# Performance work log

Measured on AMD Instinct MI355X. Metric: run time of the kernel, lower is better.

## Reference

```python
import jax, jax.numpy as jnp
import numpy as np

N_HEADS = 16
ROPE_BASE = 10000.0
EPS = float(np.finfo(np.float32).eps)  # F.rms_norm default eps for fp32


def _rms_norm(x):
    # RMSNorm over last dim, no learned scale (modded-nanogpt `norm`)
    return x * jax.lax.rsqrt(jnp.mean(jnp.square(x), axis=-1, keepdims=True) + EPS)


def _rotary(x):
    # x: [B, T, H, D]; non-interleaved half-rotation as in the Rotary module
    B, T, H, D = x.shape
    inv_freq = (1.0 / ROPE_BASE) ** (jnp.arange(0, D, 2, dtype=jnp.float32) / D)  # [D/2]
    t = jnp.arange(T, dtype=jnp.float32)
    freqs = jnp.outer(t, inv_freq)  # [T, D/2]
    cos = jnp.cos(freqs)[None, :, None, :]
    sin = jnp.sin(freqs)[None, :, None, :]
    x1, x2 = jnp.split(x, 2, axis=3)
    y1 = x1 * cos + x2 * sin
    y2 = -x1 * sin + x2 * cos
    return jnp.concatenate((y1, y2), axis=3).astype(x.dtype)


def setup_inputs() -> dict:
    key = jax.random.key(0)
    k1, k2, k3, k4 = jax.random.split(key, 4)
    B, T, Hs = 1, 2048, 2048
    d_head = Hs // N_HEADS
    std = 0.5 * d_head ** (-0.5)
    bound = 3 ** 0.5 * std
    x = jax.random.normal(k1, (B, T, Hs), dtype=jnp.float32)
    Wqkv = jax.random.uniform(k2, (3, Hs, Hs), dtype=jnp.float32, minval=-bound, maxval=bound)
    Wo_w = jax.random.normal(k3, (Hs, Hs), dtype=jnp.float32) * (Hs ** -0.5)
    Wo_b = jax.random.normal(k4, (Hs,), dtype=jnp.float32) * 0.01
    return {"x": x, "Wqkv": Wqkv, "Wo_w": Wo_w, "Wo_b": Wo_b}


def reference(x, Wqkv, Wo_w, Wo_b):
    B, T, Hs = x.shape
    d_head = Hs // N_HEADS
    # fused QKV projection: F.linear(x, Wqkv.flatten(end_dim=1)) -> x @ W^T
    W = Wqkv.reshape(3 * Hs, Hs)
    qkv = jnp.einsum('bth,oh->bto', x, W).reshape(B, T, 3 * N_HEADS, d_head)
    q, k, v = jnp.split(qkv, 3, axis=-2)  # each [B, T, H, D]
    q, k = _rms_norm(q), _rms_norm(k)
    q, k = _rotary(q), _rotary(k)
    # causal attention (flex_attention block_mask = causal), scale = 1/sqrt(d)
    scale = 1.0 / jnp.sqrt(jnp.float32(d_head))
    scores = jnp.einsum('bthd,bshd->bhts', q, k) * scale  # [B, H, T, S]
    causal = jnp.tril(jnp.ones((T, T), dtype=bool))
    scores = jnp.where(causal[None, None], scores, jnp.float32(-1e30))
    probs = jax.nn.softmax(scores, axis=-1)
    y = jnp.einsum('bhts,bshd->bthd', probs, v).reshape(B, T, Hs)
    return jnp.einsum('bth,oh->bto', y, Wo_w) + Wo_b
```

## Files before the change

kernel.cpp:

```cpp
#include <hip/hip_runtime.h>
#include <hip/hip_bf16.h>
#include <stdint.h>

#define T_SEQ 2048
#define HS    2048
#define NH    16
#define DH    128
#define QKVN  (3*HS)

typedef __attribute__((ext_vector_type(8))) short          bf16x8;
typedef __attribute__((ext_vector_type(4))) float          f32x4;
typedef __attribute__((ext_vector_type(4))) unsigned short us4;
typedef __attribute__((ext_vector_type(8))) unsigned short us8;

__device__ __forceinline__ unsigned short f2bf(float x) {
  unsigned int u = __float_as_uint(x);
  return (unsigned short)((u + 0x7fffu + ((u >> 16) & 1u)) >> 16);
}

__device__ __forceinline__ void gl_lds16(const void* g, void* l) {
  __builtin_amdgcn_global_load_lds((__attribute__((address_space(1))) void*)g,
                                   (__attribute__((address_space(3))) void*)l, 16, 0, 0);
}

__global__ __launch_bounds__(256) void cast_bf16_kernel(const float* __restrict__ in,
                                                        unsigned short* __restrict__ out, int n) {
  int i = (blockIdx.x * 256 + threadIdx.x) * 8;
  if (i >= n) return;
  f32x4 a = *(const f32x4*)(in + i);
  f32x4 b = *(const f32x4*)(in + i + 4);
  us8 r;
#pragma unroll
  for (int j = 0; j < 4; ++j) { r[j] = f2bf(a[j]); r[j + 4] = f2bf(b[j]); }
  *(us8*)(out + i) = r;
}

__global__ __launch_bounds__(256) void rope_table_kernel(float* __restrict__ cosd,
                                                         float* __restrict__ sind) {
  int i = blockIdx.x * 256 + threadIdx.x;
  if (i >= T_SEQ * 64) return;
  int t = i >> 6, f = i & 63;
  float inv = expf(-9.210340371976184f * (float)f * (1.0f / 64.0f));
  float ang = (float)t * inv;
  float s, c;
  sincosf(ang, &s, &c);
  cosd[i] = c; sind[i] = s;
}

template <int BIAS, int BN>
__global__ __launch_bounds__(256, 4)
void gemm_bt(const unsigned short* __restrict__ A, const unsigned short* __restrict__ Bt,
             float* __restrict__ C, const float* __restrict__ bias, int M, int N, int K) {
  constexpr int FN = BN / 32;
  __shared__ unsigned short As[128 * 64];
  __shared__ unsigned short Bs[BN * 64];
  const int tid  = threadIdx.x;
  const int lane = tid & 63;
  const int w    = tid >> 6;
  const int fr   = lane & 15;
  const int fq   = lane >> 4;
  const int bm   = blockIdx.y * 128;
  const int bn   = blockIdx.x * BN;
  const int wr   = (w >> 1) * 64;
  const int wc   = (w & 1) * (BN / 2);

  f32x4 acc[4][FN];
#pragma unroll
  for (int m = 0; m < 4; ++m)
#pragma unroll
    for (int n = 0; n < FN; ++n) { acc[m][n][0]=0.f; acc[m][n][1]=0.f; acc[m][n][2]=0.f; acc[m][n][3]=0.f; }

  const int srow = lane >> 3;
  const int sg   = (lane & 7) ^ srow;
  const unsigned short* Ag = A + (long)bm * K;
  const unsigned short* Bg = Bt + (long)bn * K;

  const int nk = K >> 6;
  for (int kt = 0; kt < nk; ++kt) {
    const int k0 = kt << 6;
    __syncthreads();
#pragma unroll
    for (int i = 0; i < 4; ++i) {
      int r = i * 32 + w * 8;
      gl_lds16(Ag + (long)(r + srow) * K + k0 + sg * 8, &As[r * 64]);
    }
#pragma unroll
    for (int i = 0; i < BN / 32; ++i) {
      int r = i * 32 + w * 8;
      gl_lds16(Bg + (long)(r + srow) * K + k0 + sg * 8, &Bs[r * 64]);
    }
    __syncthreads();
    __builtin_amdgcn_s_setprio(1);
#pragma unroll
    for (int ks = 0; ks < 2; ++ks) {
      bf16x8 af[4], bfr[FN];
#pragma unroll
      for (int m = 0; m < 4; ++m)
        af[m]  = *(const bf16x8*)&As[(wr + m * 16 + fr) * 64 + (((ks * 4 + fq) ^ (fr & 7)) << 3)];
#pragma unroll
      for (int n = 0; n < FN; ++n)
        bfr[n] = *(const bf16x8*)&Bs[(wc + n * 16 + fr) * 64 + (((ks * 4 + fq) ^ (fr & 7)) << 3)];
#pragma unroll
      for (int m = 0; m < 4; ++m)
#pragma unroll
        for (int n = 0; n < FN; ++n)
          acc[m][n] = __builtin_amdgcn_mfma_f32_16x16x32_bf16(af[m], bfr[n], acc[m][n], 0, 0, 0);
    }
    __builtin_amdgcn_s_setprio(0);
  }
#pragma unroll
  for (int m = 0; m < 4; ++m) {
    int row0 = bm + wr + m * 16 + fq * 4;
#pragma unroll
    for (int n = 0; n < FN; ++n) {
      int col = bn + wc + n * 16 + fr;
      float bv = BIAS ? bias[col] : 0.0f;
#pragma unroll
      for (int j = 0; j < 4; ++j)
        C[(long)(row0 + j) * N + col] = acc[m][n][j] + bv;
    }
  }
}

__global__ __launch_bounds__(256)
void normrope_qk(const float* __restrict__ qkv, const float* __restrict__ cosd,
                 const float* __restrict__ sind, unsigned short* __restrict__ qb,
                 unsigned short* __restrict__ kb) {
  const int wgl  = (blockIdx.x * 256 + threadIdx.x) >> 6;
  const int lane = threadIdx.x & 63;
  for (int rr = wgl; rr < T_SEQ * 32; rr += 4096) {
    const int t = rr >> 5;
    const int y = rr & 31;
    const float2 v = *(const float2*)(qkv + (long)t * QKVN + y * 128 + lane * 2);
    float ss = v.x * v.x + v.y * v.y;
#pragma unroll
    for (int m = 1; m < 64; m <<= 1) ss += __shfl_xor(ss, m, 64);
    const float r = rsqrtf(ss * (1.0f / 128.0f) + 1.1920928955078125e-07f);
    const float a = v.x * r, b = v.y * r;
    const float pa = __shfl_xor(a, 32, 64), pb = __shfl_xor(b, 32, 64);
    const float2 c2 = *(const float2*)(cosd + t * 64 + (lane & 31) * 2);
    const float2 s2 = *(const float2*)(sind + t * 64 + (lane & 31) * 2);
    float o0, o1;
    if (lane < 32) { o0 =  a * c2.x + pa * s2.x;  o1 =  b * c2.y + pb * s2.y; }
    else           { o0 = -pa * s2.x + a * c2.x;  o1 = -pb * s2.y + b * c2.y; }
    unsigned short* dst = (y >> 4) ? kb : qb;
    const unsigned int packed = (unsigned int)f2bf(o0) | ((unsigned int)f2bf(o1) << 16);
    *(unsigned int*)(dst + ((long)(y & 15) * T_SEQ + t) * 128 + lane * 2) = packed;
  }
}

__global__ __launch_bounds__(256)
void v_transpose(const float* __restrict__ qkv, unsigned short* __restrict__ vt) {
  const int tb = blockIdx.x;
  const int h  = blockIdx.y;
  __shared__ unsigned short vl[128][72];
  const int tid = threadIdx.x;
#pragma unroll
  for (int p = 0; p < 32; ++p) {
    int rr = p * 2 + (tid >> 7);
    int d  = tid & 127;
    float x = qkv[(long)(tb * 64 + rr) * QKVN + 2 * HS + h * 128 + d];
    vl[d][rr] = f2bf(x);
  }
  __syncthreads();
#pragma unroll
  for (int p = 0; p < 8; ++p) {
    int idx = (p * 256 + tid) * 4;
    int d = idx >> 6;
    int i = idx & 63;
    us4 val = *(const us4*)&vl[d][i];
    *(us4*)&vt[((long)h * DH + d) * T_SEQ + tb * 64 + i] = val;
  }
}

__global__ __launch_bounds__(256, 3)
void attn_kernel(const unsigned short* __restrict__ qg, const unsigned short* __restrict__ kg,
                 const unsigned short* __restrict__ vtg, float* __restrict__ accG,
                 float* __restrict__ mlG) {
  const int bi = blockIdx.x;
  const int q0 = (bi & 255) >> 4;
  const int h  = bi & 15;
  const int quarter = bi >> 8;
  const int qb = (quarter < 2) ? (31 - q0) : q0;
  const int p  = quarter & 1;
  const int slot = (qb * 16 + h) * 2 + p;

  const int kt0 = p ? ((qb >> 1) + 1) : 0;
  const int kte = p ? qb : (qb >> 1);

  const int tid = threadIdx.x, lane = tid & 63, w = tid >> 6;
  const int fr = lane & 15, fq = lane >> 4;

  float* accO = accG + (long)slot * 8192;
  float* mlO  = mlG + slot * 128;

  if (kt0 > kte) {
#pragma unroll
    for (int j3 = 0; j3 < 4; ++j3) {
      int row = w * 16 + fq * 4 + j3;
      if (fr == 0) { mlO[row] = -1e30f; mlO[64 + row] = 0.f; }
    }
    return;
  }

  __shared__ unsigned short Ks[64 * 128];
  __shared__ unsigned short Vts[128 * 64];
  __shared__ unsigned short Ps[4][16 * 72];

  const unsigned short* qh = qg  + (long)h * T_SEQ * 128;
  const unsigned short* kh = kg  + (long)h * T_SEQ * 128;
  const unsigned short* vh = vtg + (long)h * 128 * T_SEQ;

  us8 kreg[4], vreg[4];

  {
    const unsigned short* ksrc = kh + (long)kt0 * 8192;
#pragma unroll
    for (int i = 0; i < 4; ++i) {
      int gidx = tid + 256 * i;
      int row = gidx >> 4, pos = gidx & 15;
      kreg[i] = *(const us8*)(ksrc + row * 128 + pos * 8);
      int d = gidx >> 3, vpos = gidx & 7;
      vreg[i] = *(const us8*)(vh + (long)d * T_SEQ + kt0 * 64 + vpos * 8);
    }
#pragma unroll
    for (int i = 0; i < 4; ++i) {
      int gidx = tid + 256 * i;
      int row = gidx >> 4, pos = gidx & 15;
      *(us8*)&Ks[row * 128 + ((pos ^ (row & 7)) << 3)] = kreg[i];
      int d = gidx >> 3, vpos = gidx & 7;
      *(us8*)&Vts[d * 64 + ((vpos ^ (d & 7)) << 3)] = vreg[i];
    }
  }

  bf16x8 aq[4];
  {
    const unsigned short* qrow = qh + (long)(qb * 64 + w * 16 + fr) * 128;
#pragma unroll
    for (int ks = 0; ks < 4; ++ks)
      aq[ks] = *(const bf16x8*)(qrow + ks * 32 + fq * 8);
  }

  bf16x8 vone;
#pragma unroll
  for (int e = 0; e < 8; ++e) vone[e] = (short)0x3F80;

  f32x4 acc[8];
#pragma unroll
  for (int n = 0; n < 8; ++n) { acc[n][0]=0.f; acc[n][1]=0.f; acc[n][2]=0.f; acc[n][3]=0.f; }
  f32x4 accS;  accS[0]=0.f; accS[1]=0.f; accS[2]=0.f; accS[3]=0.f;
  float mrow[4];
#pragma unroll
  for (int j2 = 0; j2 < 4; ++j2) mrow[j2] = -1e30f;

  const float scale2 = 0.08838834764831845f * 1.4426950408889634f;

  __syncthreads();

  for (int kt = kt0; kt <= kte; ++kt) {
    if (kt < kte) {
      const unsigned short* ksrc = kh + (long)(kt + 1) * 8192;
#pragma unroll
      for (int i = 0; i < 4; ++i) {
        int gidx = tid + 256 * i;
        int row = gidx >> 4, pos = gidx & 15;
        kreg[i] = *(const us8*)(ksrc + row * 128 + pos * 8);
        int d = gidx >> 3, vpos = gidx & 7;
        vreg[i] = *(const us8*)(vh + (long)d * T_SEQ + (kt + 1) * 64 + vpos * 8);
      }
    }

    f32x4 sv[4];
#pragma unroll
    for (int n = 0; n < 4; ++n) { sv[n][0]=0.f; sv[n][1]=0.f; sv[n][2]=0.f; sv[n][3]=0.f; }
    __builtin_amdgcn_s_setprio(1);
#pragma unroll
    for (int ks = 0; ks < 4; ++ks)
#pragma unroll
      for (int n = 0; n < 4; ++n) {
        int R = n * 16 + fr;
        bf16x8 bk = *(const bf16x8*)&Ks[R * 128 + (((ks * 4 + fq) ^ (fr & 7)) << 3)];
        sv[n] = __builtin_amdgcn_mfma_f32_16x16x32_bf16(aq[ks], bk, sv[n], 0, 0, 0);
      }
    __builtin_amdgcn_s_setprio(0);

#pragma unroll
    for (int n = 0; n < 4; ++n)
#pragma unroll
      for (int j3 = 0; j3 < 4; ++j3) {
        float s = sv[n][j3] * scale2;
        if (kt == qb && (n * 16 + fr) > (w * 16 + fq * 4 + j3)) s = -1e30f;
        sv[n][j3] = s;
      }

    float pm[4];
#pragma unroll
    for (int j3 = 0; j3 < 4; ++j3)
      pm[j3] = fmaxf(fmaxf(sv[0][j3], sv[1][j3]), fmaxf(sv[2][j3], sv[3][j3]));
#pragma unroll
    for (int m = 1; m < 16; m <<= 1)
#pragma unroll
      for (int j3 = 0; j3 < 4; ++j3) pm[j3] = fmaxf(pm[j3], __shfl_xor(pm[j3], m, 64));

    bool grow = (pm[0] > mrow[0]) | (pm[1] > mrow[1]) | (pm[2] > mrow[2]) | (pm[3] > mrow[3]);
    if (__any(grow)) {
      float alpha[4];
#pragma unroll
      for (int j3 = 0; j3 < 4; ++j3) {
        float mn = fmaxf(mrow[j3], pm[j3]);
        alpha[j3] = exp2f(mrow[j3] - mn);
        mrow[j3] = mn;
      }
#pragma unroll
      for (int n = 0; n < 8; ++n)
#pragma unroll
        for (int j3 = 0; j3 < 4; ++j3) acc[n][j3] *= alpha[j3];
#pragma unroll
      for (int j3 = 0; j3 < 4; ++j3) accS[j3] *= alpha[j3];
    }

    unsigned short* pl = &Ps[w][0];
#pragma unroll
    for (int n = 0; n < 4; ++n)
#pragma unroll
      for (int j3 = 0; j3 < 4; ++j3)
        pl[(fq * 4 + j3) * 72 + n * 16 + fr] = f2bf(exp2f(sv[n][j3] - mrow[j3]));
    asm volatile("s_waitcnt lgkmcnt(0)" ::: "memory");
    __builtin_amdgcn_s_setprio(1);
#pragma unroll
    for (int ks = 0; ks < 2; ++ks) {
      bf16x8 pa = *(const bf16x8*)&pl[fr * 72 + ks * 32 + fq * 8];
      accS = __builtin_amdgcn_mfma_f32_16x16x32_bf16(pa, vone, accS, 0, 0, 0);
#pragma unroll
      for (int n = 0; n < 8; ++n) {
        int R = n * 16 + fr;
        bf16x8 bv = *(const bf16x8*)&Vts[R * 64 + (((ks * 4 + fq) ^ (fr & 7)) << 3)];
        acc[n] = __builtin_amdgcn_mfma_f32_16x16x32_bf16(pa, bv, acc[n], 0, 0, 0);
      }
    }
    __builtin_amdgcn_s_setprio(0);

    __syncthreads();
    if (kt < kte) {
#pragma unroll
      for (int i = 0; i < 4; ++i) {
        int gidx = tid + 256 * i;
        int row = gidx >> 4, pos = gidx & 15;
        *(us8*)&Ks[row * 128 + ((pos ^ (row & 7)) << 3)] = kreg[i];
        int d = gidx >> 3, vpos = gidx & 7;
        *(us8*)&Vts[d * 64 + ((vpos ^ (d & 7)) << 3)] = vreg[i];
      }
    }
    __syncthreads();
  }

#pragma unroll
  for (int j3 = 0; j3 < 4; ++j3) {
    int row = w * 16 + fq * 4 + j3;
#pragma unroll
    for (int n = 0; n < 8; ++n)
      accO[row * 128 + n * 16 + fr] = acc[n][j3];
    if (fr == 0) { mlO[row] = mrow[j3]; mlO[64 + row] = accS[j3]; }
  }
}

__global__ __launch_bounds__(256)
void attn_combine(const float* __restrict__ accG, const float* __restrict__ mlG,
                  unsigned short* __restrict__ yb) {
  const int j = blockIdx.x;
  const int qb = j >> 4, h = j & 15;
  const float* a0 = accG + (long)(j * 2 + 0) * 8192;
  const float* a1 = accG + (long)(j * 2 + 1) * 8192;
  const float* ml0 = mlG + (j * 2 + 0) * 128;
  const float* ml1 = mlG + (j * 2 + 1) * 128;
  const int tid = threadIdx.x;
#pragma unroll
  for (int e = 0; e < 8; ++e) {
    int idx = e * 256 + tid;
    int row = idx >> 5;
    int c4  = (idx & 31) * 4;
    float m0 = ml0[row], l0 = ml0[64 + row];
    float m1 = ml1[row], l1 = ml1[64 + row];
    float m  = fmaxf(m0, m1);
    float w0 = exp2f(m0 - m), w1 = exp2f(m1 - m);
    float inv = 1.0f / (l0 * w0 + l1 * w1);
    f32x4 A = *(const f32x4*)(a0 + row * 128 + c4);
    f32x4 B = *(const f32x4*)(a1 + row * 128 + c4);
    us4 o;
#pragma unroll
    for (int q = 0; q < 4; ++q)
      o[q] = f2bf((A[q] * w0 + B[q] * w1) * inv);
    *(us4*)(yb + (long)(qb * 64 + row) * HS + h * 128 + c4) = o;
  }
}

extern "C" void kernel_launch(void* const* d_in, const int* in_sizes, int n_in,
                              void* d_out, int out_size, void* d_ws, size_t ws_size,
                              hipStream_t stream) {
  const float* x    = (const float*)d_in[0];
  const float* Wqkv = (const float*)d_in[1];
  const float* Wo_w = (const float*)d_in[2];
  const float* Wo_b = (const float*)d_in[3];
  float* out = (float*)d_out;
  char* ws = (char*)d_ws;

  unsigned short* xbf  = (unsigned short*)(ws + 0L);
  unsigned short* wqbf = (unsigned short*)(ws + 8388608L);
  unsigned short* wobf = (unsigned short*)(ws + 33554432L);
  float*          qkv  = (float*)         (ws + 41943040L);
  unsigned short* qb   = (unsigned short*)(ws + 92274688L);
  unsigned short* kb   = (unsigned short*)(ws + 100663296L);
  unsigned short* vt   = (unsigned short*)(ws + 109051904L);
  unsigned short* yb   = (unsigned short*)(ws + 117440512L);
  float*          cosd = (float*)         (ws + 125829120L);
  float*          sind = (float*)         (ws + 126353408L);
  float*          accG = (float*)         (ws + 0L);
  float*          mlG  = (float*)         (ws + 41943040L);

  cast_bf16_kernel<<<dim3(4194304 / 8 / 256), 256, 0, stream>>>(x, xbf, 4194304);
  cast_bf16_kernel<<<dim3(12582912 / 8 / 256), 256, 0, stream>>>(Wqkv, wqbf, 12582912);
  cast_bf16_kernel<<<dim3(4194304 / 8 / 256), 256, 0, stream>>>(Wo_w, wobf, 4194304);
  rope_table_kernel<<<dim3(512), 256, 0, stream>>>(cosd, sind);

  gemm_bt<0, 128><<<dim3(QKVN / 128, T_SEQ / 128), 256, 0, stream>>>(xbf, wqbf, qkv, nullptr,
                                                                     T_SEQ, QKVN, HS);
  normrope_qk<<<dim3(1024), 256, 0, stream>>>(qkv, cosd, sind, qb, kb);
  v_transpose<<<dim3(T_SEQ / 64, NH), 256, 0, stream>>>(qkv, vt);
  attn_kernel<<<dim3(1024), 256, 0, stream>>>(qb, kb, vt, accG, mlG);
  attn_combine<<<dim3(512), 256, 0, stream>>>(accG, mlG, yb);
  gemm_bt<1, 64><<<dim3(HS / 64, T_SEQ / 128), 256, 0, stream>>>(yb, wobf, out, Wo_b,
                                                                 T_SEQ, HS, HS);
}
```

Before: 295.8 us.

## Use 128-row query tiles with 512-thread attention blocks sharing K/V tiles

The attention kernel now processes 128 query rows per block with 8 waves (512 threads) instead of 64 rows with 4 waves. Each K/V tile loaded into LDS is reused by twice as many query rows, and the split-KV partition is rebalanced so both halves of every query block are non-empty. The combine kernel is adjusted to the larger tiles. The costs are fewer blocks (512), a higher register-pressure target (launch bounds 512,4), and a causal mask that now covers two diagonal tiles.

```diff
diff --git a/kernel.cpp b/kernel.cpp
--- a/kernel.cpp
+++ b/kernel.cpp
@@ -173,69 +173,59 @@
   }
 }
 
-__global__ __launch_bounds__(256, 3)
+__global__ __launch_bounds__(512, 4)
 void attn_kernel(const unsigned short* __restrict__ qg, const unsigned short* __restrict__ kg,
                  const unsigned short* __restrict__ vtg, float* __restrict__ accG,
                  float* __restrict__ mlG) {
   const int bi = blockIdx.x;
-  const int q0 = (bi & 255) >> 4;
-  const int h  = bi & 15;
-  const int quarter = bi >> 8;
-  const int qb = (quarter < 2) ? (31 - q0) : q0;
-  const int p  = quarter & 1;
-  const int slot = (qb * 16 + h) * 2 + p;
-
-  const int kt0 = p ? ((qb >> 1) + 1) : 0;
-  const int kte = p ? qb : (qb >> 1);
+  const int j  = bi & 255;
+  const int h  = j & 15;
+  const int Q0 = j >> 4;
+  const int p  = bi >> 8;
+  const int Q  = p ? Q0 : (15 - Q0);
+  const int slot = (Q * 16 + h) * 2 + p;
+  const int kt0 = p ? (Q + 1) : 0;
+  const int kte = p ? (2 * Q + 1) : Q;
 
   const int tid = threadIdx.x, lane = tid & 63, w = tid >> 6;
   const int fr = lane & 15, fq = lane >> 4;
 
-  float* accO = accG + (long)slot * 8192;
-  float* mlO  = mlG + slot * 128;
-
-  if (kt0 > kte) {
-#pragma unroll
-    for (int j3 = 0; j3 < 4; ++j3) {
-      int row = w * 16 + fq * 4 + j3;
-      if (fr == 0) { mlO[row] = -1e30f; mlO[64 + row] = 0.f; }
-    }
-    return;
-  }
+  float* accO = accG + (long)slot * 16384;
+  float* mlO  = mlG + slot * 256;
 
   __shared__ unsigned short Ks[64 * 128];
   __shared__ unsigned short Vts[128 * 64];
-  __shared__ unsigned short Ps[4][16 * 72];
+  __shared__ unsigned short Ps[8][16 * 72];
 
   const unsigned short* qh = qg  + (long)h * T_SEQ * 128;
   const unsigned short* kh = kg  + (long)h * T_SEQ * 128;
   const unsigned short* vh = vtg + (long)h * 128 * T_SEQ;
 
-  us8 kreg[4], vreg[4];
+  us8 kreg[2], vreg[2];
 
   {
     const unsigned short* ksrc = kh + (long)kt0 * 8192;
 #pragma unroll
-    for (int i = 0; i < 4; ++i) {
-      int gidx = tid + 256 * i;
-      int row = gidx >> 4, pos = gidx & 15;
+    for (int i = 0; i < 2; ++i) {
+      int g = tid + 512 * i;
+      int row = g >> 4, pos = g & 15;
       kreg[i] = *(const us8*)(ksrc + row * 128 + pos * 8);
-      int d = gidx >> 3, vpos = gidx & 7;
+      int d = g >> 3, vpos = g & 7;
       vreg[i] = *(const us8*)(vh + (long)d * T_SEQ + kt0 * 64 + vpos * 8);
     }
 #pragma unroll
-    for (int i = 0; i < 4; ++i) {
-      int gidx = tid + 256 * i;
-      int row = gidx >> 4, pos = gidx & 15;
+    for (int i = 0; i < 2; ++i) {
+      int g = tid + 512 * i;
+      int row = g >> 4, pos = g & 15;
       *(us8*)&Ks[row * 128 + ((pos ^ (row & 7)) << 3)] = kreg[i];
-      int d = gidx >> 3, vpos = gidx & 7;
+      int d = g >> 3, vpos = g & 7;
       *(us8*)&Vts[d * 64 + ((vpos ^ (d & 7)) << 3)] = vreg[i];
     }
   }
 
   bf16x8 aq[4];
   {
-    const unsigned short* qrow = qh + (long)(qb * 64 + w * 16 + fr) * 128;
+    const unsigned short* qrow = qh + (long)(Q * 128 + w * 16 + fr) * 128;
 #pragma unroll
     for (int ks = 0; ks < 4; ++ks)
       aq[ks] = *(const bf16x8*)(qrow + ks * 32 + fq * 8);
@@ -261,11 +251,11 @@
     if (kt < kte) {
       const unsigned short* ksrc = kh + (long)(kt + 1) * 8192;
 #pragma unroll
-      for (int i = 0; i < 4; ++i) {
-        int gidx = tid + 256 * i;
-        int row = gidx >> 4, pos = gidx & 15;
+      for (int i = 0; i < 2; ++i) {
+        int g = tid + 512 * i;
+        int row = g >> 4, pos = g & 15;
         kreg[i] = *(const us8*)(ksrc + row * 128 + pos * 8);
-        int d = gidx >> 3, vpos = gidx & 7;
+        int d = g >> 3, vpos = g & 7;
         vreg[i] = *(const us8*)(vh + (long)d * T_SEQ + (kt + 1) * 64 + vpos * 8);
       }
     }
@@ -287,11 +277,17 @@
 #pragma unroll
     for (int n = 0; n < 4; ++n)
 #pragma unroll
-      for (int j3 = 0; j3 < 4; ++j3) {
-        float s = sv[n][j3] * scale2;
-        if (kt == qb && (n * 16 + fr) > (w * 16 + fq * 4 + j3)) s = -1e30f;
-        sv[n][j3] = s;
-      }
+      for (int j3 = 0; j3 < 4; ++j3) sv[n][j3] *= scale2;
+    if (kt >= (Q << 1)) {
+#pragma unroll
+      for (int n = 0; n < 4; ++n)
+#pragma unroll
+        for (int j3 = 0; j3 < 4; ++j3) {
+          int col = kt * 64 + n * 16 + fr;
+          int rowg = Q * 128 + w * 16 + fq * 4 + j3;
+          if (col > rowg) sv[n][j3] = -1e30f;
+        }
+    }
 
     float pm[4];
 #pragma unroll
@@ -343,11 +339,11 @@
     __syncthreads();
     if (kt < kte) {
 #pragma unroll
-      for (int i = 0; i < 4; ++i) {
-        int gidx = tid + 256 * i;
-        int row = gidx >> 4, pos = gidx & 15;
+      for (int i = 0; i < 2; ++i) {
+        int g = tid + 512 * i;
+        int row = g >> 4, pos = g & 15;
         *(us8*)&Ks[row * 128 + ((pos ^ (row & 7)) << 3)] = kreg[i];
-        int d = gidx >> 3, vpos = gidx & 7;
+        int d = g >> 3, vpos = g & 7;
         *(us8*)&Vts[d * 64 + ((vpos ^ (d & 7)) << 3)] = vreg[i];
       }
     }
@@ -360,7 +356,7 @@
 #pragma unroll
     for (int n = 0; n < 8; ++n)
       accO[row * 128 + n * 16 + fr] = acc[n][j3];
-    if (fr == 0) { mlO[row] = mrow[j3]; mlO[64 + row] = accS[j3]; }
+    if (fr == 0) { mlO[row] = mrow[j3]; mlO[128 + row] = accS[j3]; }
   }
 }
 
@@ -368,19 +364,19 @@
 void attn_combine(const float* __restrict__ accG, const float* __restrict__ mlG,
                   unsigned short* __restrict__ yb) {
   const int j = blockIdx.x;
-  const int qb = j >> 4, h = j & 15;
-  const float* a0 = accG + (long)(j * 2 + 0) * 8192;
-  const float* a1 = accG + (long)(j * 2 + 1) * 8192;
-  const float* ml0 = mlG + (j * 2 + 0) * 128;
-  const float* ml1 = mlG + (j * 2 + 1) * 128;
+  const int Q = j >> 4, h = j & 15;
+  const float* a0 = accG + (long)(j * 2 + 0) * 16384;
+  const float* a1 = accG + (long)(j * 2 + 1) * 16384;
+  const float* ml0 = mlG + (j * 2 + 0) * 256;
+  const float* ml1 = mlG + (j * 2 + 1) * 256;
   const int tid = threadIdx.x;
 #pragma unroll
-  for (int e = 0; e < 8; ++e) {
+  for (int e = 0; e < 16; ++e) {
     int idx = e * 256 + tid;
     int row = idx >> 5;
     int c4  = (idx & 31) * 4;
-    float m0 = ml0[row], l0 = ml0[64 + row];
-    float m1 = ml1[row], l1 = ml1[64 + row];
+    float m0 = ml0[row], l0 = ml0[128 + row];
+    float m1 = ml1[row], l1 = ml1[128 + row];
     float m  = fmaxf(m0, m1);
     float w0 = exp2f(m0 - m), w1 = exp2f(m1 - m);
     float inv = 1.0f / (l0 * w0 + l1 * w1);
@@ -390,7 +386,7 @@
 #pragma unroll
     for (int q = 0; q < 4; ++q)
       o[q] = f2bf((A[q] * w0 + B[q] * w1) * inv);
-    *(us4*)(yb + (long)(qb * 64 + row) * HS + h * 128 + c4) = o;
+    *(us4*)(yb + (long)(Q * 128 + row) * HS + h * 128 + c4) = o;
   }
 }
 
@@ -426,8 +422,8 @@
                                                                      T_SEQ, QKVN, HS);
   normrope_qk<<<dim3(1024), 256, 0, stream>>>(qkv, cosd, sind, qb, kb);
   v_transpose<<<dim3(T_SEQ / 64, NH), 256, 0, stream>>>(qkv, vt);
-  attn_kernel<<<dim3(1024), 256, 0, stream>>>(qb, kb, vt, accG, mlG);
-  attn_combine<<<dim3(512), 256, 0, stream>>>(accG, mlG, yb);
+  attn_kernel<<<dim3(512), 512, 0, stream>>>(qb, kb, vt, accG, mlG);
+  attn_combine<<<dim3(256), 256, 0, stream>>>(accG, mlG, yb);
   gemm_bt<1, 64><<<dim3(HS / 64, T_SEQ / 128), 256, 0, stream>>>(yb, wobf, out, Wo_b,
                                                                  T_SEQ, HS, HS);
 }
```

Result: no change. 301.2 us (+1.8%).
